# Kernel tuning notes

Hardware: AMD Instinct MI355X
Metric: run time of the kernel (lower is better)

The kernel has to match this reference:

```python
import jax, jax.numpy as jnp
import numpy as np

B, N, C = 2, 8192, 768
H, K = 12, 256
D = C // H
HID = 4 * C
EPS = 1e-6

def layer_norm(x, w, b):
    mu = jnp.mean(x, axis=-1, keepdims=True)
    var = jnp.mean(jnp.square(x - mu), axis=-1, keepdims=True)
    return (x - mu) * jax.lax.rsqrt(var + EPS) * w + b

def setup_inputs() -> dict:
    key = jax.random.key(0)
    ks = jax.random.split(key, 8)
    s = 0.02
    return {
        "x": jax.random.normal(ks[0], (B, N, C), jnp.float32),
        "ln1_w": jnp.ones((C,), jnp.float32),
        "ln1_b": jnp.zeros((C,), jnp.float32),
        "qkv_w": jax.random.normal(ks[1], (C, 3 * C), jnp.float32) * s,
        "qkv_b": jnp.zeros((3 * C,), jnp.float32),
        "Ek": jax.random.normal(ks[2], (N, K), jnp.float32) * s,
        "Ev": jax.random.normal(ks[3], (N, K), jnp.float32) * s,
        "proj_w": jax.random.normal(ks[4], (C, C), jnp.float32) * s,
        "proj_b": jnp.zeros((C,), jnp.float32),
        "ln2_w": jnp.ones((C,), jnp.float32),
        "ln2_b": jnp.zeros((C,), jnp.float32),
        "fc1_w": jax.random.normal(ks[5], (C, HID), jnp.float32) * s,
        "fc1_b": jnp.zeros((HID,), jnp.float32),
        "fc2_w": jax.random.normal(ks[6], (HID, C), jnp.float32) * s,
        "fc2_b": jnp.zeros((C,), jnp.float32),
    }

def reference(x, ln1_w, ln1_b, qkv_w, qkv_b, Ek, Ev, proj_w, proj_b,
              ln2_w, ln2_b, fc1_w, fc1_b, fc2_w, fc2_b):
    scale = D ** -0.5
    # --- attention branch ---
    h = layer_norm(x, ln1_w, ln1_b)
    qkv = h @ qkv_w + qkv_b                      # (B,N,3C)
    qkv = qkv.reshape(B, N, 3, H, D).transpose(2, 0, 3, 1, 4)  # (3,B,H,N,D)
    q, k, v = qkv[0], qkv[1], qkv[2]
    # Linformer: project K/V along sequence dim N -> K
    k_proj = jnp.einsum('bhnd,nk->bhkd', k, Ek)
    v_proj = jnp.einsum('bhnd,nk->bhkd', v, Ev)
    logits = jnp.einsum('bhnd,bhkd->bhnk', q, k_proj) * scale
    logits = jnp.clip(logits, -50.0, 50.0)
    attn = jax.nn.softmax(logits, axis=-1)
    o = jnp.einsum('bhnk,bhkd->bhnd', attn, v_proj)
    o = o.transpose(0, 2, 1, 3).reshape(B, N, C)
    o = o @ proj_w + proj_b
    x = x + o                                    # alpha_attn = 1.0
    # --- MLP branch ---
    h = layer_norm(x, ln2_w, ln2_b)
    h = jax.nn.gelu(h @ fc1_w + fc1_b, approximate=False)
    h = h @ fc2_w + fc2_b
    return x + h                                 # alpha_mlp = 1.0
```

## Files before the change

kernel.cpp:

```cpp
#include <hip/hip_runtime.h>
#include <cstdint>

#define DEV __device__ __forceinline__

typedef __bf16 bf16x8 __attribute__((ext_vector_type(8)));
typedef float f32x4 __attribute__((ext_vector_type(4)));

DEV uint16_t f2bf(float f) {
  uint32_t u = __float_as_uint(f);
  u += 0x7FFFu + ((u >> 16) & 1u);
  return (uint16_t)(u >> 16);
}
DEV float bf2f(uint16_t h) { return __uint_as_float(((uint32_t)h) << 16); }

DEV void gload16(const void* g, void* l) {
  __builtin_amdgcn_global_load_lds((const __attribute__((address_space(1))) void*)g,
                                   (__attribute__((address_space(3))) void*)l, 16, 0, 0);
}

template <int N> DEV void waitcnt_vm() {
  if constexpr (N == 0) asm volatile("s_waitcnt vmcnt(0)" ::: "memory");
  else if constexpr (N == 4) asm volatile("s_waitcnt vmcnt(4)" ::: "memory");
  else static_assert(N == 0 || N == 4, "unsupported vmcnt");
}

DEV float gelu_f(float v) {
  float u = v * (0.7978845608f + 0.0356774081f * v * v);
  return v / (1.f + __expf(-2.f * u));
}

__global__ __launch_bounds__(256) void ln768(const float* __restrict__ x,
                                             const float* __restrict__ w,
                                             const float* __restrict__ b,
                                             uint16_t* __restrict__ out) {
  const size_t row = blockIdx.x;
  const float* xr = x + row * 768;
  const int t = threadIdx.x;
  float v0 = xr[t], v1 = xr[t + 256], v2 = xr[t + 512];
  float s = v0 + v1 + v2;
  float s2 = v0 * v0 + v1 * v1 + v2 * v2;
#pragma unroll
  for (int o = 32; o; o >>= 1) {
    s += __shfl_down(s, o);
    s2 += __shfl_down(s2, o);
  }
  __shared__ float sh[8];
  if ((t & 63) == 0) { sh[t >> 6] = s; sh[4 + (t >> 6)] = s2; }
  __syncthreads();
  s = sh[0] + sh[1] + sh[2] + sh[3];
  s2 = sh[4] + sh[5] + sh[6] + sh[7];
  const float mu = s * (1.f / 768.f);
  const float var = s2 * (1.f / 768.f) - mu * mu;
  const float rstd = rsqrtf(var + 1e-6f);
  uint16_t* orow = out + row * 768;
  orow[t]       = f2bf((v0 - mu) * rstd * w[t] + b[t]);
  orow[t + 256] = f2bf((v1 - mu) * rstd * w[t + 256] + b[t + 256]);
  orow[t + 512] = f2bf((v2 - mu) * rstd * w[t + 512] + b[t + 512]);
}

__global__ __launch_bounds__(256) void transpose_f2b(const float* __restrict__ in,
                                                     uint16_t* __restrict__ outp,
                                                     int ldin, int ldout) {
  __shared__ float tile[32][33];
  const int tx = threadIdx.x, ty = threadIdx.y;
  const size_t x = (size_t)blockIdx.x * 32 + tx;
  const size_t y = (size_t)blockIdx.y * 32 + ty;
#pragma unroll
  for (int j = 0; j < 4; ++j) tile[ty + j * 8][tx] = in[(y + j * 8) * ldin + x];
  __syncthreads();
  const size_t x2 = (size_t)blockIdx.y * 32 + tx;
  const size_t y2 = (size_t)blockIdx.x * 32 + ty;
#pragma unroll
  for (int j = 0; j < 4; ++j) outp[(y2 + j * 8) * ldout + x2] = f2bf(tile[tx][ty + j * 8]);
}

__global__ __launch_bounds__(256) void transpose_b2b(const uint16_t* __restrict__ in,
                                                     uint16_t* __restrict__ outp,
                                                     int ldin, int ldout) {
  __shared__ uint16_t tile[32][33];
  const int tx = threadIdx.x, ty = threadIdx.y;
  const size_t x = (size_t)blockIdx.x * 32 + tx;
  const size_t y = (size_t)blockIdx.y * 32 + ty;
#pragma unroll
  for (int j = 0; j < 4; ++j) tile[ty + j * 8][tx] = in[(y + j * 8) * ldin + x];
  __syncthreads();
  const size_t x2 = (size_t)blockIdx.y * 32 + tx;
  const size_t y2 = (size_t)blockIdx.x * 32 + ty;
#pragma unroll
  for (int j = 0; j < 4; ++j) outp[(y2 + j * 8) * ldout + x2] = tile[tx][ty + j * 8];
}

__global__ __launch_bounds__(256) void kv_tn(const uint16_t* __restrict__ EkT,
                                             const uint16_t* __restrict__ EvT,
                                             const uint16_t* __restrict__ qkv,
                                             float* __restrict__ part) {
  const int bid = blockIdx.x;
  const int wg = (bid & 7) * 96 + (bid >> 3);
  const int inner = wg & 15;
  const int kt = inner & 3, ns = inner >> 2;
  const int rest = wg >> 4;
  const int ct = rest % 12, kvb = rest / 12;
  const int kv = kvb >> 1, b = kvb & 1;
  const int k0 = kt * 64, c0 = ct * 64, nsb = ns * 2048;

  const uint16_t* E = kv ? EvT : EkT;
  const uint16_t* KV = qkv + (size_t)b * 8192 * 2304 + 768 + kv * 768 + c0;
  const int tid = threadIdx.x, wave = tid >> 6, lane = tid & 63;
  const int l16 = lane & 15, lhi = lane >> 4;
  const int wm = wave >> 1, wn = wave & 1;

  f32x4 acc[2][2];
#pragma unroll
  for (int m = 0; m < 2; ++m)
#pragma unroll
    for (int n = 0; n < 2; ++n) acc[m][n] = f32x4{0.f, 0.f, 0.f, 0.f};

  const uint16_t* Eb = E + (size_t)(k0 + wm * 32 + l16) * 8192 + nsb + lhi * 8;
  const uint16_t* KVb = KV + ((size_t)nsb + lhi * 8) * 2304 + wn * 32 + l16;

  for (int n0 = 0; n0 < 2048; n0 += 32) {
    bf16x8 ef[2];
    ef[0] = *(const bf16x8*)(Eb + n0);
    ef[1] = *(const bf16x8*)(Eb + 16 * 8192 + n0);
    bf16x8 vf[2];
#pragma unroll
    for (int nf = 0; nf < 2; ++nf) {
      const uint16_t* p = KVb + (size_t)n0 * 2304 + nf * 16;
      union { bf16x8 v; uint16_t u[8]; } tu;
#pragma unroll
      for (int j = 0; j < 8; ++j) tu.u[j] = p[(size_t)j * 2304];
      vf[nf] = tu.v;
    }
#pragma unroll
    for (int m = 0; m < 2; ++m)
#pragma unroll
      for (int nf = 0; nf < 2; ++nf)
        acc[m][nf] = __builtin_amdgcn_mfma_f32_16x16x32_bf16(ef[m], vf[nf], acc[m][nf], 0, 0, 0);
  }

  float* outp = part + ((size_t)ns * 4 + kvb) * 196608;
#pragma unroll
  for (int m = 0; m < 2; ++m)
#pragma unroll
    for (int nf = 0; nf < 2; ++nf)
#pragma unroll
      for (int r = 0; r < 4; ++r)
        outp[(size_t)(k0 + wm * 32 + m * 16 + lhi * 4 + r) * 768 + c0 + wn * 32 + nf * 16 + l16] =
            acc[m][nf][r];
}

__global__ __launch_bounds__(256) void kv_reduce(const float* __restrict__ part,
                                                 uint16_t* __restrict__ kproj) {
  const int kvb = blockIdx.y;
  const int i = blockIdx.x * 256 + threadIdx.x;
  const float* p = part + (size_t)kvb * 196608 + i;
  float s = p[0] + p[786432] + p[2 * 786432] + p[3 * 786432];
  kproj[(size_t)kvb * 196608 + i] = f2bf(s);
}

__global__ __launch_bounds__(256, 3) void attn_fused(
    const uint16_t* __restrict__ qkv, const uint16_t* __restrict__ kproj,
    const uint16_t* __restrict__ vprojT, uint16_t* __restrict__ o) {
  const int bh = blockIdx.y;
  const int b = bh / 12, h = bh % 12;
  const int n0 = blockIdx.x * 64;
  const int tid = threadIdx.x, wave = tid >> 6, lane = tid & 63;
  const int l16 = lane & 15, lhi = lane >> 4;
  const int wm = wave >> 1, wn = wave & 1;

  __shared__ __align__(16) uint16_t sP[64 * 256];
  __shared__ float redm[2][64], reds[2][64], recs[64];

  const uint16_t* Kp = kproj + (size_t)b * 196608 + h * 64;
  const uint16_t* Qp = qkv + ((size_t)b * 8192 + n0) * 2304 + h * 64;
  const uint16_t* Vp = vprojT + ((size_t)b * 768 + h * 64) * 256;

  f32x4 st[8][2];
#pragma unroll
  for (int m = 0; m < 8; ++m)
#pragma unroll
    for (int nf = 0; nf < 2; ++nf) st[m][nf] = f32x4{0.f, 0.f, 0.f, 0.f};
#pragma unroll
  for (int ks = 0; ks < 2; ++ks) {
    bf16x8 kf[8], qf[2];
#pragma unroll
    for (int m = 0; m < 8; ++m) {
      const int kvi = wm * 128 + m * 16 + l16;
      kf[m] = *(const bf16x8*)(Kp + (size_t)kvi * 768 + ks * 32 + lhi * 8);
    }
#pragma unroll
    for (int nf = 0; nf < 2; ++nf) {
      const int n = wn * 32 + nf * 16 + l16;
      qf[nf] = *(const bf16x8*)(Qp + (size_t)n * 2304 + ks * 32 + lhi * 8);
    }
#pragma unroll
    for (int m = 0; m < 8; ++m)
#pragma unroll
      for (int nf = 0; nf < 2; ++nf)
        st[m][nf] = __builtin_amdgcn_mfma_f32_16x16x32_bf16(kf[m], qf[nf], st[m][nf], 0, 0, 0);
  }

  float pmax[2] = {-50.f, -50.f};
#pragma unroll
  for (int m = 0; m < 8; ++m)
#pragma unroll
    for (int nf = 0; nf < 2; ++nf)
#pragma unroll
      for (int r = 0; r < 4; ++r) {
        float v = fminf(fmaxf(st[m][nf][r] * 0.125f, -50.f), 50.f);
        st[m][nf][r] = v;
        pmax[nf] = fmaxf(pmax[nf], v);
      }
#pragma unroll
  for (int nf = 0; nf < 2; ++nf) {
    pmax[nf] = fmaxf(pmax[nf], __shfl_xor(pmax[nf], 16));
    pmax[nf] = fmaxf(pmax[nf], __shfl_xor(pmax[nf], 32));
  }
  if (lhi == 0) {
#pragma unroll
    for (int nf = 0; nf < 2; ++nf) redm[wm][wn * 32 + nf * 16 + l16] = pmax[nf];
  }
  __syncthreads();
  float M[2];
#pragma unroll
  for (int nf = 0; nf < 2; ++nf) {
    const int col = wn * 32 + nf * 16 + l16;
    M[nf] = fmaxf(redm[0][col], redm[1][col]);
  }

  float psum[2] = {0.f, 0.f};
#pragma unroll
  for (int m = 0; m < 8; ++m) {
#pragma unroll
    for (int nf = 0; nf < 2; ++nf) {
      float e0 = __expf(st[m][nf][0] - M[nf]);
      float e1 = __expf(st[m][nf][1] - M[nf]);
      float e2 = __expf(st[m][nf][2] - M[nf]);
      float e3 = __expf(st[m][nf][3] - M[nf]);
      psum[nf] += (e0 + e1) + (e2 + e3);
      uint2 pk;
      pk.x = (uint32_t)f2bf(e0) | ((uint32_t)f2bf(e1) << 16);
      pk.y = (uint32_t)f2bf(e2) | ((uint32_t)f2bf(e3) << 16);
      const int n = wn * 32 + nf * 16 + l16;
      const int kvb2 = (wm * 128 + m * 16 + lhi * 4) * 2;
      *(uint2*)((char*)sP + n * 512 + (kvb2 ^ ((n & 7) << 4))) = pk;
    }
  }
#pragma unroll
  for (int nf = 0; nf < 2; ++nf) {
    psum[nf] += __shfl_xor(psum[nf], 16);
    psum[nf] += __shfl_xor(psum[nf], 32);
  }
  if (lhi == 0) {
#pragma unroll
    for (int nf = 0; nf < 2; ++nf) reds[wm][wn * 32 + nf * 16 + l16] = psum[nf];
  }
  __syncthreads();
  if (wm == 0 && lhi == 0) {
#pragma unroll
    for (int nf = 0; nf < 2; ++nf) {
      const int col = wn * 32 + nf * 16 + l16;
      recs[col] = 1.f / (reds[0][col] + reds[1][col]);
    }
  }
  __syncthreads();

  f32x4 pacc[2][2];
#pragma unroll
  for (int mf = 0; mf < 2; ++mf)
#pragma unroll
    for (int nf = 0; nf < 2; ++nf) pacc[mf][nf] = f32x4{0.f, 0.f, 0.f, 0.f};
#pragma unroll
  for (int ks = 0; ks < 8; ++ks) {
    bf16x8 pa[2], vb[2];
#pragma unroll
    for (int mf = 0; mf < 2; ++mf) {
      const int n = wm * 32 + mf * 16 + l16;
      pa[mf] = *(const bf16x8*)((char*)sP + n * 512 + ((ks * 64 + lhi * 16) ^ ((n & 7) << 4)));
    }
#pragma unroll
    for (int nf = 0; nf < 2; ++nf) {
      const int d = wn * 32 + nf * 16 + l16;
      vb[nf] = *(const bf16x8*)(Vp + (size_t)d * 256 + ks * 32 + lhi * 8);
    }
#pragma unroll
    for (int mf = 0; mf < 2; ++mf)
#pragma unroll
      for (int nf = 0; nf < 2; ++nf)
        pacc[mf][nf] = __builtin_amdgcn_mfma_f32_16x16x32_bf16(pa[mf], vb[nf], pacc[mf][nf], 0, 0, 0);
  }
  uint16_t* orow = o + ((size_t)b * 8192 + n0) * 768 + h * 64;
#pragma unroll
  for (int mf = 0; mf < 2; ++mf) {
#pragma unroll
    for (int r = 0; r < 4; ++r) {
      const int n = wm * 32 + mf * 16 + lhi * 4 + r;
      const float inv = recs[n];
#pragma unroll
      for (int nf = 0; nf < 2; ++nf) {
        const int d = wn * 32 + nf * 16 + l16;
        orow[(size_t)n * 768 + d] = f2bf(pacc[mf][nf][r] * inv);
      }
    }
  }
}

template <bool OUTBF, bool HASBIAS, bool DOGELU, bool HASRES>
__global__ __launch_bounds__(256, 3) void gemm128(
    const uint16_t* __restrict__ A, const uint16_t* __restrict__ B,
    void* __restrict__ Cbase, const float* __restrict__ bias,
    const float* __restrict__ res, int Kd, int lda, int ldb, int ldc) {
  constexpr int PL = 4096;
  __shared__ __align__(16) uint16_t lds[3 * 2 * PL];

  const int nn = gridDim.y;
  const int nwg = gridDim.x * gridDim.y;
  const int bid = blockIdx.y * gridDim.x + blockIdx.x;
  const int q = nwg >> 3, r8 = nwg & 7, xcd = bid & 7, idx = bid >> 3;
  const int wg = (xcd < r8 ? xcd * (q + 1) : r8 * (q + 1) + (xcd - r8) * q) + idx;
  const int bm = wg / nn, bn = wg % nn;
  const int row0 = bm * 128, col0 = bn * 128;

  const int tid = threadIdx.x;
  const int wave = tid >> 6, lane = tid & 63;
  const int wm = wave >> 1, wn = wave & 1;
  const int l16 = lane & 15, lhi = lane >> 4;
  const int srow = tid >> 2, sq = tid & 3;

  auto stage = [&](int buf, int t) {
    const int k0 = t * 32;
    uint16_t* sa = lds + buf * 2 * PL;
#pragma unroll
    for (int j = 0; j < 2; ++j) {
      const int rw = j * 64 + srow;
      const int sl = sq ^ ((rw >> 1) & 3);
      gload16(A + (size_t)(row0 + rw) * lda + k0 + sl * 8, sa + rw * 32 + sq * 8);
    }
#pragma unroll
    for (int j = 0; j < 2; ++j) {
      const int rw = j * 64 + srow;
      const int sl = sq ^ ((rw >> 1) & 3);
      gload16(B + (size_t)(col0 + rw) * ldb + k0 + sl * 8, sa + PL + rw * 32 + sq * 8);
    }
  };

  f32x4 acc[4][4];
#pragma unroll
  for (int m = 0; m < 4; ++m)
#pragma unroll
    for (int n = 0; n < 4; ++n) acc[m][n] = f32x4{0.f, 0.f, 0.f, 0.f};

  const int NT = Kd >> 5;
  stage(0, 0);
  stage(1, 1);

  for (int t = 0; t < NT; ++t) {
    if (t < NT - 1) waitcnt_vm<4>();
    else waitcnt_vm<0>();
    __builtin_amdgcn_s_barrier();
    asm volatile("" ::: "memory");
    if (t + 2 < NT) stage((t + 2) % 3, t + 2);

    const uint16_t* sa = lds + (t % 3) * 2 * PL;
    const uint16_t* sb = sa + PL;
    bf16x8 af[4], bfv[4];
#pragma unroll
    for (int n = 0; n < 4; ++n) {
      const int rw = wn * 64 + n * 16 + l16;
      bfv[n] = *(const bf16x8*)(sb + rw * 32 + (lhi ^ ((rw >> 1) & 3)) * 8);
    }
#pragma unroll
    for (int m = 0; m < 4; ++m) {
      const int rw = wm * 64 + m * 16 + l16;
      af[m] = *(const bf16x8*)(sa + rw * 32 + (lhi ^ ((rw >> 1) & 3)) * 8);
    }
    __builtin_amdgcn_s_setprio(1);
#pragma unroll
    for (int m = 0; m < 4; ++m)
#pragma unroll
      for (int n = 0; n < 4; ++n)
        acc[m][n] = __builtin_amdgcn_mfma_f32_16x16x32_bf16(af[m], bfv[n], acc[m][n], 0, 0, 0);
    __builtin_amdgcn_s_setprio(0);
  }

  float* Cf = (float*)Cbase;
  uint16_t* Cb = (uint16_t*)Cbase;
#pragma unroll
  for (int m = 0; m < 4; ++m) {
#pragma unroll
    for (int n = 0; n < 4; ++n) {
      const int col = col0 + wn * 64 + n * 16 + l16;
      float bv = 0.f;
      if (HASBIAS) bv = bias[col];
#pragma unroll
      for (int r = 0; r < 4; ++r) {
        const int row = row0 + wm * 64 + m * 16 + lhi * 4 + r;
        float v = acc[m][n][r] + bv;
        if (DOGELU) v = gelu_f(v);
        const size_t cidx = (size_t)row * ldc + col;
        if (HASRES) v += res[cidx];
        if (OUTBF) Cb[cidx] = f2bf(v);
        else Cf[cidx] = v;
      }
    }
  }
}

extern "C" void kernel_launch(void* const* d_in, const int* in_sizes, int n_in,
                              void* d_out, int out_size, void* d_ws, size_t ws_size,
                              hipStream_t stream) {
  const float* x      = (const float*)d_in[0];
  const float* ln1_w  = (const float*)d_in[1];
  const float* ln1_b  = (const float*)d_in[2];
  const float* qkv_w  = (const float*)d_in[3];
  const float* qkv_b  = (const float*)d_in[4];
  const float* Ek     = (const float*)d_in[5];
  const float* Ev     = (const float*)d_in[6];
  const float* proj_w = (const float*)d_in[7];
  const float* proj_b = (const float*)d_in[8];
  const float* ln2_w  = (const float*)d_in[9];
  const float* ln2_b  = (const float*)d_in[10];
  const float* fc1_w  = (const float*)d_in[11];
  const float* fc1_b  = (const float*)d_in[12];
  const float* fc2_w  = (const float*)d_in[13];
  const float* fc2_b  = (const float*)d_in[14];
  float* out = (float*)d_out;

  char* w8 = (char*)d_ws;
  size_t off = 0;
  auto take = [&](size_t bytes) { char* p = w8 + off; off += bytes; return p; };
  uint16_t* qkv_wT  = (uint16_t*)take(2304ull * 768 * 2);
  uint16_t* proj_wT = (uint16_t*)take(768ull * 768 * 2);
  uint16_t* fc1_wT  = (uint16_t*)take(3072ull * 768 * 2);
  uint16_t* fc2_wT  = (uint16_t*)take(768ull * 3072 * 2);
  uint16_t* EkT     = (uint16_t*)take(256ull * 8192 * 2);
  uint16_t* EvT     = (uint16_t*)take(256ull * 8192 * 2);
  uint16_t* h_bf    = (uint16_t*)take(16384ull * 768 * 2);
  uint16_t* qkv_bf  = (uint16_t*)take(16384ull * 2304 * 2);
  uint16_t* big     = (uint16_t*)take(100663296ull);
  uint16_t* kproj   = (uint16_t*)take(2ull * 2 * 256 * 768 * 2);
  uint16_t* vprojT  = (uint16_t*)take(2ull * 768 * 256 * 2);
  uint16_t* o_bf    = (uint16_t*)take(16384ull * 768 * 2);
  float* part = (float*)big;
  (void)ws_size; (void)in_sizes; (void)n_in; (void)out_size;

  const dim3 tb(32, 8);
  transpose_f2b<<<dim3(72, 24), tb, 0, stream>>>(qkv_w, qkv_wT, 2304, 768);
  transpose_f2b<<<dim3(24, 24), tb, 0, stream>>>(proj_w, proj_wT, 768, 768);
  transpose_f2b<<<dim3(96, 24), tb, 0, stream>>>(fc1_w, fc1_wT, 3072, 768);
  transpose_f2b<<<dim3(24, 96), tb, 0, stream>>>(fc2_w, fc2_wT, 768, 3072);
  transpose_f2b<<<dim3(8, 256), tb, 0, stream>>>(Ek, EkT, 256, 8192);
  transpose_f2b<<<dim3(8, 256), tb, 0, stream>>>(Ev, EvT, 256, 8192);
  ln768<<<16384, 256, 0, stream>>>(x, ln1_w, ln1_b, h_bf);
  gemm128<true, true, false, false><<<dim3(128, 18), 256, 0, stream>>>(
      h_bf, qkv_wT, qkv_bf, qkv_b, nullptr, 768, 768, 768, 2304);
  kv_tn<<<768, 256, 0, stream>>>(EkT, EvT, qkv_bf, part);
  kv_reduce<<<dim3(768, 4), 256, 0, stream>>>(part, kproj);
  for (int b = 0; b < 2; ++b)
    transpose_b2b<<<dim3(24, 8), tb, 0, stream>>>(
        kproj + (size_t)(2 + b) * 196608, vprojT + (size_t)b * 768 * 256, 768, 256);
  attn_fused<<<dim3(128, 24), 256, 0, stream>>>(qkv_bf, kproj, vprojT, o_bf);
  gemm128<false, true, false, true><<<dim3(128, 6), 256, 0, stream>>>(
      o_bf, proj_wT, out, proj_b, x, 768, 768, 768, 768);
  ln768<<<16384, 256, 0, stream>>>(out, ln2_w, ln2_b, h_bf);
  gemm128<true, true, true, false><<<dim3(128, 24), 256, 0, stream>>>(
      h_bf, fc1_wT, big, fc1_b, nullptr, 768, 768, 768, 3072);
  gemm128<false, true, false, true><<<dim3(128, 6), 256, 0, stream>>>(
      big, fc2_wT, out, fc2_b, out, 3072, 3072, 3072, 768);
}
```

Baseline: 514.0 us.

## Reassociate Linformer K/V projection through QKV weights and use 256-row MLP GEMMs

```diff
diff --git a/kernel.cpp b/kernel.cpp
--- a/kernel.cpp
+++ b/kernel.cpp
@@ -21,7 +21,8 @@
 template <int N> DEV void waitcnt_vm() {
   if constexpr (N == 0) asm volatile("s_waitcnt vmcnt(0)" ::: "memory");
   else if constexpr (N == 4) asm volatile("s_waitcnt vmcnt(4)" ::: "memory");
-  else static_assert(N == 0 || N == 4, "unsupported vmcnt");
+  else if constexpr (N == 6) asm volatile("s_waitcnt vmcnt(6)" ::: "memory");
+  else static_assert(N == 0 || N == 4 || N == 6, "unsupported vmcnt");
 }
 
 DEV float gelu_f(float v) {
@@ -90,77 +91,124 @@
   for (int j = 0; j < 4; ++j) outp[(y2 + j * 8) * ldout + x2] = tile[tx][ty + j * 8];
 }
 
-__global__ __launch_bounds__(256) void kv_tn(const uint16_t* __restrict__ EkT,
-                                             const uint16_t* __restrict__ EvT,
-                                             const uint16_t* __restrict__ qkv,
-                                             float* __restrict__ part) {
-  const int bid = blockIdx.x;
-  const int wg = (bid & 7) * 96 + (bid >> 3);
-  const int inner = wg & 15;
-  const int kt = inner & 3, ns = inner >> 2;
-  const int rest = wg >> 4;
-  const int ct = rest % 12, kvb = rest / 12;
-  const int kv = kvb >> 1, b = kvb & 1;
-  const int k0 = kt * 64, c0 = ct * 64, nsb = ns * 2048;
-
-  const uint16_t* E = kv ? EvT : EkT;
-  const uint16_t* KV = qkv + (size_t)b * 8192 * 2304 + 768 + kv * 768 + c0;
-  const int tid = threadIdx.x, wave = tid >> 6, lane = tid & 63;
+__global__ __launch_bounds__(256) void rowsum512(const uint16_t* __restrict__ ekv,
+                                                 float* __restrict__ colsum) {
+  const int row = blockIdx.x * 4 + (threadIdx.x >> 6);
+  const int lane = threadIdx.x & 63;
+  const uint16_t* r = ekv + (size_t)row * 8192 + lane * 8;
+  float s = 0.f;
+#pragma unroll
+  for (int it = 0; it < 16; ++it) {
+    bf16x8 v = *(const bf16x8*)(r + it * 512);
+#pragma unroll
+    for (int j = 0; j < 8; ++j) s += (float)v[j];
+  }
+#pragma unroll
+  for (int o = 32; o; o >>= 1) s += __shfl_down(s, o);
+  if (lane == 0) colsum[row] = s;
+}
+
+__global__ __launch_bounds__(256) void kv_reduce(const float* __restrict__ part,
+                                                 uint16_t* __restrict__ hkv) {
+  const int i = blockIdx.x * 256 + threadIdx.x;
+  float s = part[i] + part[786432 + i] + part[2 * 786432 + i] + part[3 * 786432 + i];
+  hkv[i] = f2bf(s);
+}
+
+template <int BM, int BN, bool OUTBF, bool HASBIAS, bool DOGELU, bool HASRES, bool HASRS>
+__global__ __launch_bounds__(256) void gemm_nt(
+    const uint16_t* __restrict__ Abase, const uint16_t* __restrict__ Bbase,
+    void* __restrict__ Cbase, const float* __restrict__ bias,
+    const float* __restrict__ resbase, const float* __restrict__ rowscale,
+    int Kd, int lda, int ldb, int ldc,
+    int zdiv, size_t sAhi, size_t sAlo, size_t sBhi, size_t sBlo,
+    size_t sChi, size_t sClo, int rs_z, int bias_z) {
+  const int z = blockIdx.z;
+  const int zhi = z / zdiv, zlo = z - zhi * zdiv;
+  const uint16_t* A = Abase + zhi * sAhi + zlo * sAlo;
+  const uint16_t* B = Bbase + zhi * sBhi + zlo * sBlo;
+  const size_t coff = zhi * sChi + zlo * sClo;
+
+  constexpr int WTM = BM / 2, WTN = BN / 2;
+  constexpr int FM = WTM / 16, FN = WTN / 16;
+  const int tid = threadIdx.x;
+  const int wave = tid >> 6, lane = tid & 63;
+  const int wm = wave >> 1, wn = wave & 1;
   const int l16 = lane & 15, lhi = lane >> 4;
-  const int wm = wave >> 1, wn = wave & 1;
-
-  f32x4 acc[2][2];
-#pragma unroll
-  for (int m = 0; m < 2; ++m)
-#pragma unroll
-    for (int n = 0; n < 2; ++n) acc[m][n] = f32x4{0.f, 0.f, 0.f, 0.f};
-
-  const uint16_t* Eb = E + (size_t)(k0 + wm * 32 + l16) * 8192 + nsb + lhi * 8;
-  const uint16_t* KVb = KV + ((size_t)nsb + lhi * 8) * 2304 + wn * 32 + l16;
-
-  for (int n0 = 0; n0 < 2048; n0 += 32) {
-    bf16x8 ef[2];
-    ef[0] = *(const bf16x8*)(Eb + n0);
-    ef[1] = *(const bf16x8*)(Eb + 16 * 8192 + n0);
-    bf16x8 vf[2];
-#pragma unroll
-    for (int nf = 0; nf < 2; ++nf) {
-      const uint16_t* p = KVb + (size_t)n0 * 2304 + nf * 16;
-      union { bf16x8 v; uint16_t u[8]; } tu;
-#pragma unroll
-      for (int j = 0; j < 8; ++j) tu.u[j] = p[(size_t)j * 2304];
-      vf[nf] = tu.v;
-    }
-#pragma unroll
-    for (int m = 0; m < 2; ++m)
-#pragma unroll
-      for (int nf = 0; nf < 2; ++nf)
-        acc[m][nf] = __builtin_amdgcn_mfma_f32_16x16x32_bf16(ef[m], vf[nf], acc[m][nf], 0, 0, 0);
-  }
-
-  float* outp = part + ((size_t)ns * 4 + kvb) * 196608;
-#pragma unroll
-  for (int m = 0; m < 2; ++m)
-#pragma unroll
-    for (int nf = 0; nf < 2; ++nf)
-#pragma unroll
-      for (int r = 0; r < 4; ++r)
-        outp[(size_t)(k0 + wm * 32 + m * 16 + lhi * 4 + r) * 768 + c0 + wn * 32 + nf * 16 + l16] =
-            acc[m][nf][r];
-}
-
-__global__ __launch_bounds__(256) void kv_reduce(const float* __restrict__ part,
-                                                 uint16_t* __restrict__ kproj) {
-  const int kvb = blockIdx.y;
-  const int i = blockIdx.x * 256 + threadIdx.x;
-  const float* p = part + (size_t)kvb * 196608 + i;
-  float s = p[0] + p[786432] + p[2 * 786432] + p[3 * 786432];
-  kproj[(size_t)kvb * 196608 + i] = f2bf(s);
+
+  __shared__ __align__(16) uint16_t sA[BM * 32];
+  __shared__ __align__(16) uint16_t sB[BN * 32];
+
+  f32x4 acc[FM][FN];
+#pragma unroll
+  for (int m = 0; m < FM; ++m)
+#pragma unroll
+    for (int n = 0; n < FN; ++n) acc[m][n] = f32x4{0.f, 0.f, 0.f, 0.f};
+
+  const int row0 = blockIdx.x * BM;
+  const int col0 = blockIdx.y * BN;
+  const int rr = tid >> 2, cq = tid & 3;
+
+  for (int k0 = 0; k0 < Kd; k0 += 32) {
+    __syncthreads();
+#pragma unroll
+    for (int is = 0; is < BM / 64; ++is) {
+      const uint16_t* g = A + (size_t)(row0 + is * 64 + rr) * lda + k0 + cq * 8;
+      gload16(g, &sA[is * 2048 + tid * 8]);
+    }
+#pragma unroll
+    for (int is = 0; is < BN / 64; ++is) {
+      const uint16_t* g = B + (size_t)(col0 + is * 64 + rr) * ldb + k0 + cq * 8;
+      gload16(g, &sB[is * 2048 + tid * 8]);
+    }
+    __syncthreads();
+
+    bf16x8 af[FM], bq[FN];
+#pragma unroll
+    for (int m = 0; m < FM; ++m)
+      af[m] = *(const bf16x8*)(&sA[(wm * WTM + m * 16 + l16) * 32 + lhi * 8]);
+#pragma unroll
+    for (int n = 0; n < FN; ++n)
+      bq[n] = *(const bf16x8*)(&sB[(wn * WTN + n * 16 + l16) * 32 + lhi * 8]);
+#pragma unroll
+    for (int m = 0; m < FM; ++m)
+#pragma unroll
+      for (int n = 0; n < FN; ++n)
+        acc[m][n] = __builtin_amdgcn_mfma_f32_16x16x32_bf16(af[m], bq[n], acc[m][n], 0, 0, 0);
+  }
+
+  float* Cf = (float*)Cbase;
+  uint16_t* Cb = (uint16_t*)Cbase;
+#pragma unroll
+  for (int m = 0; m < FM; ++m) {
+#pragma unroll
+    for (int n = 0; n < FN; ++n) {
+      const int col = col0 + wn * WTN + n * 16 + l16;
+      float bv = 0.f;
+      if (HASBIAS) bv = bias[zlo * bias_z + col];
+#pragma unroll
+      for (int r = 0; r < 4; ++r) {
+        const int row = row0 + wm * WTM + m * 16 + lhi * 4 + r;
+        float v = acc[m][n][r];
+        if (HASBIAS) {
+          if (HASRS) v += rowscale[zlo * rs_z + row] * bv;
+          else v += bv;
+        }
+        if (DOGELU) v = gelu_f(v);
+        const size_t cidx = coff + (size_t)row * ldc + col;
+        if (HASRES) v += resbase[cidx];
+        if (OUTBF) Cb[cidx] = f2bf(v);
+        else Cf[cidx] = v;
+      }
+    }
+  }
 }
 
 __global__ __launch_bounds__(256, 3) void attn_fused(
-    const uint16_t* __restrict__ qkv, const uint16_t* __restrict__ kproj,
-    const uint16_t* __restrict__ vprojT, uint16_t* __restrict__ o) {
+    const uint16_t* __restrict__ q,
+    const uint16_t* __restrict__ kproj,
+    const uint16_t* __restrict__ vprojT,
+    uint16_t* __restrict__ o) {
   const int bh = blockIdx.y;
   const int b = bh / 12, h = bh % 12;
   const int n0 = blockIdx.x * 64;
@@ -172,7 +220,7 @@
   __shared__ float redm[2][64], reds[2][64], recs[64];
 
   const uint16_t* Kp = kproj + (size_t)b * 196608 + h * 64;
-  const uint16_t* Qp = qkv + ((size_t)b * 8192 + n0) * 2304 + h * 64;
+  const uint16_t* Qp = q + ((size_t)b * 8192 + n0) * 768 + h * 64;
   const uint16_t* Vp = vprojT + ((size_t)b * 768 + h * 64) * 256;
 
   f32x4 st[8][2];
@@ -191,7 +239,7 @@
 #pragma unroll
     for (int nf = 0; nf < 2; ++nf) {
       const int n = wn * 32 + nf * 16 + l16;
-      qf[nf] = *(const bf16x8*)(Qp + (size_t)n * 2304 + ks * 32 + lhi * 8);
+      qf[nf] = *(const bf16x8*)(Qp + (size_t)n * 768 + ks * 32 + lhi * 8);
     }
 #pragma unroll
     for (int m = 0; m < 8; ++m)
@@ -395,6 +443,107 @@
 #pragma unroll
       for (int r = 0; r < 4; ++r) {
         const int row = row0 + wm * 64 + m * 16 + lhi * 4 + r;
+        float v = acc[m][n][r] + bv;
+        if (DOGELU) v = gelu_f(v);
+        const size_t cidx = (size_t)row * ldc + col;
+        if (HASRES) v += res[cidx];
+        if (OUTBF) Cb[cidx] = f2bf(v);
+        else Cf[cidx] = v;
+      }
+    }
+  }
+}
+
+template <bool OUTBF, bool HASBIAS, bool DOGELU, bool HASRES>
+__global__ __launch_bounds__(256, 2) void gemm256n(
+    const uint16_t* __restrict__ A, const uint16_t* __restrict__ B,
+    void* __restrict__ Cbase, const float* __restrict__ bias,
+    const float* __restrict__ res, int Kd, int lda, int ldb, int ldc) {
+  constexpr int APL = 8192, BPL = 4096;
+  __shared__ __align__(16) uint16_t lds[3 * (APL + BPL)];
+
+  const int nn = gridDim.y;
+  const int nwg = gridDim.x * gridDim.y;
+  const int bid = blockIdx.y * gridDim.x + blockIdx.x;
+  const int q = nwg >> 3, r8 = nwg & 7, xcd = bid & 7, idx = bid >> 3;
+  const int wg = (xcd < r8 ? xcd * (q + 1) : r8 * (q + 1) + (xcd - r8) * q) + idx;
+  const int bm = wg / nn, bn = wg % nn;
+  const int row0 = bm * 256, col0 = bn * 128;
+
+  const int tid = threadIdx.x;
+  const int wave = tid >> 6, lane = tid & 63;
+  const int wm = wave >> 1, wn = wave & 1;
+  const int l16 = lane & 15, lhi = lane >> 4;
+  const int srow = tid >> 2, sq = tid & 3;
+
+  auto stage = [&](int buf, int t) {
+    const int k0 = t * 32;
+    uint16_t* sa = lds + buf * (APL + BPL);
+#pragma unroll
+    for (int j = 0; j < 4; ++j) {
+      const int rw = j * 64 + srow;
+      const int sl = sq ^ ((rw >> 1) & 3);
+      gload16(A + (size_t)(row0 + rw) * lda + k0 + sl * 8, sa + rw * 32 + sq * 8);
+    }
+#pragma unroll
+    for (int j = 0; j < 2; ++j) {
+      const int rw = j * 64 + srow;
+      const int sl = sq ^ ((rw >> 1) & 3);
+      gload16(B + (size_t)(col0 + rw) * ldb + k0 + sl * 8, sa + APL + rw * 32 + sq * 8);
+    }
+  };
+
+  f32x4 acc[8][4];
+#pragma unroll
+  for (int m = 0; m < 8; ++m)
+#pragma unroll
+    for (int n = 0; n < 4; ++n) acc[m][n] = f32x4{0.f, 0.f, 0.f, 0.f};
+
+  const int NT = Kd >> 5;
+  stage(0, 0);
+  stage(1, 1);
+
+  for (int t = 0; t < NT; ++t) {
+    if (t < NT - 1) waitcnt_vm<6>();
+    else waitcnt_vm<0>();
+    __builtin_amdgcn_s_barrier();
+    asm volatile("" ::: "memory");
+    if (t + 2 < NT) stage((t + 2) % 3, t + 2);
+
+    const uint16_t* sa = lds + (t % 3) * (APL + BPL);
+    const uint16_t* sb = sa + APL;
+    bf16x8 af[8], bfv[4];
+#pragma unroll
+    for (int n = 0; n < 4; ++n) {
+      const int rw = wn * 64 + n * 16 + l16;
+      bfv[n] = *(const bf16x8*)(sb + rw * 32 + (lhi ^ ((rw >> 1) & 3)) * 8);
+    }
+#pragma unroll
+    for (int m = 0; m < 8; ++m) {
+      const int rw = wm * 128 + m * 16 + l16;
+      af[m] = *(const bf16x8*)(sa + rw * 32 + (lhi ^ ((rw >> 1) & 3)) * 8);
+    }
+    __builtin_amdgcn_s_setprio(1);
+#pragma unroll
+    for (int m = 0; m < 8; ++m)
+#pragma unroll
+      for (int n = 0; n < 4; ++n)
+        acc[m][n] = __builtin_amdgcn_mfma_f32_16x16x32_bf16(af[m], bfv[n], acc[m][n], 0, 0, 0);
+    __builtin_amdgcn_s_setprio(0);
+  }
+
+  float* Cf = (float*)Cbase;
+  uint16_t* Cb = (uint16_t*)Cbase;
+#pragma unroll
+  for (int m = 0; m < 8; ++m) {
+#pragma unroll
+    for (int n = 0; n < 4; ++n) {
+      const int col = col0 + wn * 64 + n * 16 + l16;
+      float bv = 0.f;
+      if (HASBIAS) bv = bias[col];
+#pragma unroll
+      for (int r = 0; r < 4; ++r) {
+        const int row = row0 + wm * 128 + m * 16 + lhi * 4 + r;
         float v = acc[m][n][r] + bv;
         if (DOGELU) v = gelu_f(v);
         const size_t cidx = (size_t)row * ldc + col;
@@ -436,11 +585,14 @@
   uint16_t* EkT     = (uint16_t*)take(256ull * 8192 * 2);
   uint16_t* EvT     = (uint16_t*)take(256ull * 8192 * 2);
   uint16_t* h_bf    = (uint16_t*)take(16384ull * 768 * 2);
-  uint16_t* qkv_bf  = (uint16_t*)take(16384ull * 2304 * 2);
+  uint16_t* hT      = (uint16_t*)take(2ull * 768 * 8192 * 2);
+  uint16_t* q_bf    = (uint16_t*)take(16384ull * 768 * 2);
   uint16_t* big     = (uint16_t*)take(100663296ull);
-  uint16_t* kproj   = (uint16_t*)take(2ull * 2 * 256 * 768 * 2);
+  uint16_t* hkv_bf  = (uint16_t*)take(2ull * 512 * 768 * 2);
+  uint16_t* kproj   = (uint16_t*)take(4ull * 256 * 768 * 2);
   uint16_t* vprojT  = (uint16_t*)take(2ull * 768 * 256 * 2);
   uint16_t* o_bf    = (uint16_t*)take(16384ull * 768 * 2);
+  float* colsum     = (float*)take(512 * 4);
   float* part = (float*)big;
   (void)ws_size; (void)in_sizes; (void)n_in; (void)out_size;
 
@@ -452,19 +604,29 @@
   transpose_f2b<<<dim3(8, 256), tb, 0, stream>>>(Ek, EkT, 256, 8192);
   transpose_f2b<<<dim3(8, 256), tb, 0, stream>>>(Ev, EvT, 256, 8192);
   ln768<<<16384, 256, 0, stream>>>(x, ln1_w, ln1_b, h_bf);
-  gemm128<true, true, false, false><<<dim3(128, 18), 256, 0, stream>>>(
-      h_bf, qkv_wT, qkv_bf, qkv_b, nullptr, 768, 768, 768, 2304);
-  kv_tn<<<768, 256, 0, stream>>>(EkT, EvT, qkv_bf, part);
-  kv_reduce<<<dim3(768, 4), 256, 0, stream>>>(part, kproj);
+  for (int b = 0; b < 2; ++b)
+    transpose_b2b<<<dim3(24, 256), tb, 0, stream>>>(
+        h_bf + (size_t)b * 8192 * 768, hT + (size_t)b * 768 * 8192, 768, 8192);
+  rowsum512<<<128, 256, 0, stream>>>(EkT, colsum);
+  gemm128<true, true, false, false><<<dim3(128, 6), 256, 0, stream>>>(
+      h_bf, qkv_wT, q_bf, qkv_b, nullptr, 768, 768, 768, 768);
+  gemm_nt<64, 64, false, false, false, false, false><<<dim3(8, 12, 8), 256, 0, stream>>>(
+      EkT, hT, part, nullptr, nullptr, nullptr, 2048, 8192, 8192, 768,
+      4, 0, 2048, 768ull * 8192, 2048, 393216, 786432, 0, 0);
+  kv_reduce<<<3072, 256, 0, stream>>>(part, hkv_bf);
+  gemm_nt<64, 64, true, true, false, false, true><<<dim3(4, 12, 4), 256, 0, stream>>>(
+      hkv_bf, qkv_wT + 768ull * 768, kproj, qkv_b + 768, nullptr, colsum,
+      768, 768, 768, 768,
+      2, 512ull * 768, 256ull * 768, 0, 768ull * 768, 196608, 393216, 256, 768);
   for (int b = 0; b < 2; ++b)
     transpose_b2b<<<dim3(24, 8), tb, 0, stream>>>(
         kproj + (size_t)(2 + b) * 196608, vprojT + (size_t)b * 768 * 256, 768, 256);
-  attn_fused<<<dim3(128, 24), 256, 0, stream>>>(qkv_bf, kproj, vprojT, o_bf);
+  attn_fused<<<dim3(128, 24), 256, 0, stream>>>(q_bf, kproj, vprojT, o_bf);
   gemm128<false, true, false, true><<<dim3(128, 6), 256, 0, stream>>>(
       o_bf, proj_wT, out, proj_b, x, 768, 768, 768, 768);
   ln768<<<16384, 256, 0, stream>>>(out, ln2_w, ln2_b, h_bf);
-  gemm128<true, true, true, false><<<dim3(128, 24), 256, 0, stream>>>(
+  gemm256n<true, true, true, false><<<dim3(64, 24), 256, 0, stream>>>(
       h_bf, fc1_wT, big, fc1_b, nullptr, 768, 768, 768, 3072);
-  gemm128<false, true, false, true><<<dim3(128, 6), 256, 0, stream>>>(
+  gemm256n<false, true, false, true><<<dim3(64, 6), 256, 0, stream>>>(
       big, fc2_wT, out, fc2_b, out, 3072, 3072, 3072, 768);
 }
```

Result: faster. 473.3 us (-7.9%).
